# Performance work log

Hardware: AMD Instinct MI355X
Metric: run time of the kernel (lower is better)

## Reference

```python
import jax, jax.numpy as jnp
import numpy as np

N_NODES = 100000
IN_CH, HID_CH, OUT_CH = 128, 128, 64
N_EDGES = 1600000


def _gcn_conv(x, W, b, src, dst, num_nodes):
    """PyG GCNConv with gcn_norm(add_self_loops=True): adds one self-loop per
    node to the given edge set, symmetric deg^-1/2 normalization, then
    gather-scale-scatter of the linearly transformed features."""
    loop = jnp.arange(num_nodes)
    s = jnp.concatenate([src, loop])
    d = jnp.concatenate([dst, loop])
    # degree over targets (flow source_to_target), edge weights = 1
    deg = jax.ops.segment_sum(jnp.ones_like(s, x.dtype), d, num_segments=num_nodes)
    dinv = jnp.where(deg > 0, deg ** -0.5, 0.0)
    norm = dinv[s] * dinv[d]                      # [E']
    h = x @ W                                     # [N, out]
    msg = h[s] * norm[:, None]                    # [E', out] gather + scale
    out = jax.ops.segment_sum(msg, d, num_segments=num_nodes)  # scatter-add
    return out + b


def setup_inputs() -> dict:
    key = jax.random.key(0)
    k = jax.random.split(key, 6)
    x = jax.random.normal(k[0], (N_NODES, IN_CH), dtype=jnp.float32)
    edge_index = jax.random.randint(k[1], (2, N_EDGES), 0, N_NODES, dtype=jnp.int64)
    # Glorot-scale params
    W1 = jax.random.normal(k[2], (IN_CH, HID_CH), dtype=jnp.float32) * (2.0 / (IN_CH + HID_CH)) ** 0.5
    b1 = jnp.zeros((HID_CH,), dtype=jnp.float32)
    W2 = jax.random.normal(k[3], (HID_CH, OUT_CH), dtype=jnp.float32) * (2.0 / (HID_CH + OUT_CH)) ** 0.5
    b2 = jnp.zeros((OUT_CH,), dtype=jnp.float32)
    return {"x": x, "edge_index": edge_index, "W1": W1, "b1": b1, "W2": W2, "b2": b2}


def reference(x, edge_index, W1, b1, W2, b2):
    num_nodes = x.shape[0]
    loop = jnp.arange(num_nodes, dtype=edge_index.dtype)
    # wrapper-level add_self_loops (GCNConv adds another internally)
    src = jnp.concatenate([edge_index[0], loop])
    dst = jnp.concatenate([edge_index[1], loop])
    h = _gcn_conv(x, W1, b1, src, dst, num_nodes)
    h = jax.nn.relu(h)
    h = _gcn_conv(h, W2, b2, src, dst, num_nodes)
    return jax.nn.log_softmax(h, axis=1)
```

## Files before the change

### kernel.cpp

```cpp
#include <hip/hip_runtime.h>
#include <cstdint>
#include <cstddef>

#define IN_CH 128
#define HID_CH 128
#define OUT_CH 64
#define BSH 8
#define PB 4096
#define CAP 6144

typedef unsigned int uint32;
typedef unsigned char uchar;
typedef short bf16x8 __attribute__((ext_vector_type(8)));
typedef float f32x4 __attribute__((ext_vector_type(4)));
typedef float f32x2 __attribute__((ext_vector_type(2)));

static __device__ __forceinline__ unsigned short f2bf(float f) {
    uint32 u = __float_as_uint(f);
    u += 0x7fffu + ((u >> 16) & 1u);
    return (unsigned short)(u >> 16);
}

typedef const __attribute__((address_space(1))) char gch;
typedef __attribute__((address_space(3))) char lch;
static __device__ __forceinline__ void gload16(const void* g, void* l) {
    __builtin_amdgcn_global_load_lds((gch*)g, (lch*)l, 16, 0, 0);
}


__global__ __launch_bounds__(256) void part1_wtrans(
    const int* __restrict__ src, const int* __restrict__ dst,
    int* __restrict__ bcur, int2* __restrict__ pairBuf, int E, int NB, int gP,
    const float* __restrict__ W1, const float* __restrict__ W2,
    unsigned short* __restrict__ W1t, unsigned short* __restrict__ W2t) {
    if (blockIdx.x >= (uint32)gP) {
        int t = (blockIdx.x - gP) * 256 + threadIdx.x;
        if (t < 128 * 128) {
            int nc = t >> 7, k = t & 127;
            W1t[t] = f2bf(W1[k * 128 + nc]);
        }
        int u = t - 128 * 128;
        if (u >= 0 && u < 64 * 128) {
            int nc = u >> 7, k = u & 127;
            W2t[u] = f2bf(W2[k * 64 + nc]);
        }
        return;
    }
    __shared__ int2 pairs[PB];
    __shared__ int hist[512];
    __shared__ int base[512];
    int t = threadIdx.x;
    int e0 = blockIdx.x * PB;
    int cnt = min(PB, E - e0);
    for (int b = t; b < NB; b += 256) hist[b] = 0;
    __syncthreads();
    for (int i = t; i < cnt; i += 256) {
        int s = src[e0 + i], d = dst[e0 + i];
        pairs[i] = make_int2(s, d);
        atomicAdd(&hist[d >> BSH], 1);
    }
    __syncthreads();
    for (int b = t; b < NB; b += 256) {
        int h = hist[b];
        int gb = (h > 0) ? atomicAdd(&bcur[b], h) : 0;
        base[b] = b * CAP + gb;
        hist[b] = 0;
    }
    __syncthreads();
    for (int i = t; i < cnt; i += 256) {
        int2 p = pairs[i];
        int b = p.y >> BSH;
        int q = base[b] + atomicAdd(&hist[b], 1);
        pairBuf[q] = p;
    }
}

__global__ __launch_bounds__(256) void bucket_build(
    const int2* __restrict__ pairBuf, const int* __restrict__ bcur,
    int* __restrict__ rowptr, int* __restrict__ deg, float* __restrict__ dinv,
    int* __restrict__ csr, int N) {
    __shared__ int cnt[256];
    __shared__ int loc[256];
    int b = blockIdx.x, t = threadIdx.x;
    int start = b * CAP, end = start + bcur[b];
    cnt[t] = 0;
    __syncthreads();
    for (int i = start + t; i < end; i += 256)
        atomicAdd(&cnt[pairBuf[i].y & 255], 1);
    __syncthreads();
    int v = cnt[t];
    loc[t] = v;
    __syncthreads();
    for (int o = 1; o < 256; o <<= 1) {
        int add = (t >= o) ? loc[t - o] : 0;
        __syncthreads();
        loc[t] += add;
        __syncthreads();
    }
    int excl = loc[t] - v;
    int node = (b << BSH) + t;
    if (node < N) {
        rowptr[node] = start + excl;
        deg[node] = v;
        dinv[node] = rsqrtf((float)(v + 2));
    }
    __syncthreads();
    cnt[t] = excl;
    __syncthreads();
    for (int i = start + t; i < end; i += 256) {
        int2 p = pairBuf[i];
        int q = start + atomicAdd(&cnt[p.y & 255], 1);
        csr[q] = p.x;
    }
}


__global__ __launch_bounds__(256) void gemm1_mfma(
    const float* __restrict__ A, const unsigned short* __restrict__ Wt,
    const float* __restrict__ dinv, uchar* __restrict__ C, int n, int nTiles) {
    constexpr int NT = 8;
    __shared__ unsigned short Ws[128 * 136];
    __shared__ char As[64 * 512];

    const int t = threadIdx.x;

    for (int i = t; i < 128 * 16; i += 256) {
        int rr = i >> 4, sq = i & 15;
        *(uint4*)&Ws[rr * 136 + sq * 8] = *(const uint4*)(Wt + rr * 128 + sq * 8);
    }

    const int w = t >> 6, l = t & 63;
    const int q = l >> 4, r16 = l & 15;
    const int rw = w * 16 + r16;

    for (int tile = blockIdx.x; tile < nTiles; tile += gridDim.x) {
        const int row0 = tile * 64;

#pragma unroll
        for (int rnd = 0; rnd < 8; rnd++) {
            int p = rnd * 4096 + t * 16;
            int row = row0 + (p >> 9);
            int col = p & 511;
            gload16((const char*)A + (size_t)min(row, n - 1) * 512 + col, As + p);
        }
        __syncthreads();

        f32x4 acc[NT];
#pragma unroll
        for (int i = 0; i < NT; i++) acc[i] = (f32x4){0.f, 0.f, 0.f, 0.f};

#pragma unroll
        for (int s = 0; s < 4; s++) {
            const int k0 = s * 32 + q * 8;
            const float* Arow = (const float*)(As + rw * 512);
            float4 v0 = *(const float4*)(Arow + k0);
            float4 v1 = *(const float4*)(Arow + k0 + 4);
            bf16x8 xf;
            xf[0] = (short)f2bf(v0.x); xf[1] = (short)f2bf(v0.y);
            xf[2] = (short)f2bf(v0.z); xf[3] = (short)f2bf(v0.w);
            xf[4] = (short)f2bf(v1.x); xf[5] = (short)f2bf(v1.y);
            xf[6] = (short)f2bf(v1.z); xf[7] = (short)f2bf(v1.w);
#pragma unroll
            for (int nt = 0; nt < NT; nt++) {
                bf16x8 wf = *(const bf16x8*)&Ws[(nt * 16 + r16) * 136 + k0];
                acc[nt] = __builtin_amdgcn_mfma_f32_16x16x32_bf16(wf, xf, acc[nt], 0, 0, 0);
            }
        }

        const int node = row0 + rw;
        const bool nv = node < n;
        const float dv = dinv[min(node, n - 1)];
        uchar* Crow = C + (size_t)node * 128;
#pragma unroll
        for (int nt = 0; nt < NT; nt++) {
            int pk = 0;
            pk = __builtin_amdgcn_cvt_pk_fp8_f32(acc[nt][0] * dv, acc[nt][1] * dv, pk, false);
            pk = __builtin_amdgcn_cvt_pk_fp8_f32(acc[nt][2] * dv, acc[nt][3] * dv, pk, true);
            if (nv) *(uint32*)(Crow + nt * 16 + q * 4) = (uint32)pk;
        }
        __syncthreads();
    }
}


__global__ __launch_bounds__(256) void agg1_fused(
    const uchar* __restrict__ H, const int* __restrict__ csr,
    const int* __restrict__ rowptr, const int* __restrict__ deg,
    const float* __restrict__ dinv, const float* __restrict__ bias,
    const unsigned short* __restrict__ W2t, uchar* __restrict__ H2, int n) {
    __shared__ char stage[4][8192];
    __shared__ unsigned short tile[16 * 136];
    int t = threadIdx.x;
    int slot = t >> 4;
    int v = blockIdx.x * 16 + slot;
    int hl = t & 15;
    int gsel = t & 48;
    int w = t >> 6;
    int gg = (t >> 4) & 3;
    bool valid = v < n;
    int vc = valid ? v : 0;
    int base = rowptr[vc];
    int cnt = valid ? deg[vc] : 0;

    f32x2 A0 = (f32x2){0.f, 0.f}, A1 = A0, A2 = A0, A3 = A0;
    f32x2 B0 = A0, B1 = A0, B2 = A0, B3 = A0;

#define ACC128(h, s0, s1, s2, s3)                                   \
    {                                                               \
        s0 += __builtin_amdgcn_cvt_pk_f32_fp8((h).x, false);        \
        s1 += __builtin_amdgcn_cvt_pk_f32_fp8((h).x, true);         \
        s2 += __builtin_amdgcn_cvt_pk_f32_fp8((h).y, false);        \
        s3 += __builtin_amdgcn_cvt_pk_f32_fp8((h).y, true);         \
    }

    char* sl = stage[w];
    const char* rg = sl + gg * 256 + hl * 8;

    int ul = 0;
    if (hl < min(16, cnt)) ul = csr[base + hl];

    for (int j0 = 0; j0 < cnt; j0 += 16) {
        int nj = min(16, cnt - j0);
#pragma unroll
        for (int i = 0; i < 8; i++) {
            int j = i * 2 + (hl >> 3);
            int u = __shfl(ul, j | gsel);
            gload16(H + (((uint32)u << 7) + ((uint32)(hl & 7) << 4)),
                    sl + i * 1024);
        }
        int ul2 = 0;
        int j0n = j0 + 16;
        if (j0n < cnt && hl < min(16, cnt - j0n)) ul2 = csr[base + j0n + hl];
        asm volatile("s_waitcnt vmcnt(4)" ::: "memory");
        __builtin_amdgcn_sched_barrier(0);
#pragma unroll
        for (int j = 0; j < 8; j++) {
            if (j < nj) {
                uint2 h = *(const uint2*)(rg + (j >> 1) * 1024 + (j & 1) * 128);
                if (j & 1) { ACC128(h, B0, B1, B2, B3); }
                else       { ACC128(h, A0, A1, A2, A3); }
            }
        }
        asm volatile("s_waitcnt vmcnt(0)" ::: "memory");
        __builtin_amdgcn_sched_barrier(0);
#pragma unroll
        for (int j = 8; j < 16; j++) {
            if (j < nj) {
                uint2 h = *(const uint2*)(rg + (j >> 1) * 1024 + (j & 1) * 128);
                if (j & 1) { ACC128(h, B0, B1, B2, B3); }
                else       { ACC128(h, A0, A1, A2, A3); }
            }
        }
        ul = ul2;
    }
#undef ACC128

    const uint32 co = (uint32)(hl * 8);
    uint4 pk = make_uint4(0, 0, 0, 0);
    if (valid) {
        float dv = dinv[vc];
        uint2 hv = *(const uint2*)(H + (((uint32)vc << 7) + co));
        f32x2 s0 = __builtin_amdgcn_cvt_pk_f32_fp8(hv.x, false);
        f32x2 s1 = __builtin_amdgcn_cvt_pk_f32_fp8(hv.x, true);
        f32x2 s2 = __builtin_amdgcn_cvt_pk_f32_fp8(hv.y, false);
        f32x2 s3 = __builtin_amdgcn_cvt_pk_f32_fp8(hv.y, true);
        const f32x2* bp = (const f32x2*)(bias + hl * 8);
        f32x2 e0 = dv * ((A0 + B0) + 2.f * s0) + bp[0];
        f32x2 e1 = dv * ((A1 + B1) + 2.f * s1) + bp[1];
        f32x2 e2 = dv * ((A2 + B2) + 2.f * s2) + bp[2];
        f32x2 e3 = dv * ((A3 + B3) + 2.f * s3) + bp[3];
        float o0 = fmaxf(e0[0], 0.f), o1 = fmaxf(e0[1], 0.f);
        float o2 = fmaxf(e1[0], 0.f), o3 = fmaxf(e1[1], 0.f);
        float o4 = fmaxf(e2[0], 0.f), o5 = fmaxf(e2[1], 0.f);
        float o6 = fmaxf(e3[0], 0.f), o7 = fmaxf(e3[1], 0.f);
        pk.x = (uint32)f2bf(o0) | ((uint32)f2bf(o1) << 16);
        pk.y = (uint32)f2bf(o2) | ((uint32)f2bf(o3) << 16);
        pk.z = (uint32)f2bf(o4) | ((uint32)f2bf(o5) << 16);
        pk.w = (uint32)f2bf(o6) | ((uint32)f2bf(o7) << 16);
    }
    *(uint4*)&tile[slot * 136 + hl * 8] = pk;
    __syncthreads();

    const int l = t & 63;
    const int q = l >> 4, r16 = l & 15;
    f32x4 acc2 = (f32x4){0.f, 0.f, 0.f, 0.f};
#pragma unroll
    for (int s = 0; s < 4; s++) {
        const int k0 = s * 32 + q * 8;
        bf16x8 hf = *(const bf16x8*)&tile[r16 * 136 + k0];
        bf16x8 wf = *(const bf16x8*)(W2t + (size_t)(w * 16 + r16) * 128 + k0);
        acc2 = __builtin_amdgcn_mfma_f32_16x16x32_bf16(wf, hf, acc2, 0, 0, 0);
    }
    const int node = blockIdx.x * 16 + r16;
    if (node < n) {
        const float dv2 = dinv[node];
        int pk2 = 0;
        pk2 = __builtin_amdgcn_cvt_pk_fp8_f32(acc2[0] * dv2, acc2[1] * dv2, pk2, false);
        pk2 = __builtin_amdgcn_cvt_pk_fp8_f32(acc2[2] * dv2, acc2[3] * dv2, pk2, true);
        *(uint32*)(H2 + (size_t)node * 64 + w * 16 + q * 4) = (uint32)pk2;
    }
}

__global__ __launch_bounds__(256) void agg_lsm_64(
    const uchar* __restrict__ H, const int* __restrict__ csr,
    const int* __restrict__ rowptr, const int* __restrict__ deg,
    const float* __restrict__ dinv, const float* __restrict__ bias,
    float* __restrict__ out, int n) {
    __shared__ char stage[4][4096];
    int t = threadIdx.x;
    int v = blockIdx.x * 16 + (t >> 4);
    int hl = t & 15;
    int gsel = t & 48;
    int w = t >> 6;
    int gg = (t >> 4) & 3;
    bool valid = v < n;
    int vc = valid ? v : 0;
    int base = rowptr[vc];
    int cnt = valid ? deg[vc] : 0;
    const uint32 co = (uint32)(hl * 4);

    f32x2 A0 = (f32x2){0.f, 0.f}, A1 = A0, B0 = A0, B1 = A0;

#define ACC64(h, s0, s1)                                            \
    {                                                               \
        s0 += __builtin_amdgcn_cvt_pk_f32_fp8((h), false);          \
        s1 += __builtin_amdgcn_cvt_pk_f32_fp8((h), true);           \
    }

    char* sl = stage[w];
    const char* rg = sl + gg * 256 + hl * 4;

    int ul = 0;
    if (hl < min(16, cnt)) ul = csr[base + hl];

    for (int j0 = 0; j0 < cnt; j0 += 16) {
        int nj = min(16, cnt - j0);
#pragma unroll
        for (int i = 0; i < 4; i++) {
            int j = i * 4 + (hl >> 2);
            int u = __shfl(ul, j | gsel);
            gload16(H + (((uint32)u << 6) + ((uint32)(hl & 3) << 4)),
                    sl + i * 1024);
        }
        int ul2 = 0;
        int j0n = j0 + 16;
        if (j0n < cnt && hl < min(16, cnt - j0n)) ul2 = csr[base + j0n + hl];
        asm volatile("s_waitcnt vmcnt(2)" ::: "memory");
        __builtin_amdgcn_sched_barrier(0);
#pragma unroll
        for (int j = 0; j < 8; j++) {
            if (j < nj) {
                uint32 h = *(const uint32*)(rg + (j >> 2) * 1024 + (j & 3) * 64);
                if (j & 1) { ACC64(h, B0, B1); }
                else       { ACC64(h, A0, A1); }
            }
        }
        asm volatile("s_waitcnt vmcnt(0)" ::: "memory");
        __builtin_amdgcn_sched_barrier(0);
#pragma unroll
        for (int j = 8; j < 16; j++) {
            if (j < nj) {
                uint32 h = *(const uint32*)(rg + (j >> 2) * 1024 + (j & 3) * 64);
                if (j & 1) { ACC64(h, B0, B1); }
                else       { ACC64(h, A0, A1); }
            }
        }
        ul = ul2;
    }
#undef ACC64

    float dv = dinv[vc];
    uint32 hv = *(const uint32*)(H + (((uint32)vc << 6) + co));
    f32x2 s0 = __builtin_amdgcn_cvt_pk_f32_fp8(hv, false);
    f32x2 s1 = __builtin_amdgcn_cvt_pk_f32_fp8(hv, true);
    const f32x2* bp = (const f32x2*)(bias + hl * 4);
    f32x2 w0 = dv * ((A0 + B0) + 2.f * s0) + bp[0];
    f32x2 w1 = dv * ((A1 + B1) + 2.f * s1) + bp[1];
    float v0 = w0[0], v1 = w0[1], v2 = w1[0], v3 = w1[1];
    float m = fmaxf(fmaxf(v0, v1), fmaxf(v2, v3));
    for (int o = 8; o > 0; o >>= 1) m = fmaxf(m, __shfl_xor(m, o));
    float e = (__expf(v0 - m) + __expf(v1 - m)) + (__expf(v2 - m) + __expf(v3 - m));
    for (int o = 8; o > 0; o >>= 1) e += __shfl_xor(e, o);
    float ls = m + __logf(e);
    if (valid)
        *(float4*)(out + (size_t)vc * 64 + hl * 4) =
            make_float4(v0 - ls, v1 - ls, v2 - ls, v3 - ls);
}


extern "C" void kernel_launch(void* const* d_in, const int* in_sizes, int n_in,
                              void* d_out, int out_size, void* d_ws, size_t ws_size,
                              hipStream_t stream) {
    const float* x  = (const float*)d_in[0];
    const int*   ei = (const int*)d_in[1];
    const float* W1 = (const float*)d_in[2];
    const float* b1 = (const float*)d_in[3];
    const float* W2 = (const float*)d_in[4];
    const float* b2 = (const float*)d_in[5];
    float* out = (float*)d_out;

    const int N = in_sizes[0] / IN_CH;
    const int E = in_sizes[1] / 2;
    const int* src = ei;
    const int* dst = ei + E;
    const int NB = (N + 255) >> BSH;

    char* w = (char*)d_ws;
    size_t off = 0;
    auto alloc = [&](size_t bytes) -> char* {
        char* p = w + off;
        off = (off + bytes + 255) & ~(size_t)255;
        return p;
    };
    int*   deg    = (int*)alloc((size_t)N * 4);
    int*   rowptr = (int*)alloc((size_t)N * 4);
    int*   bcur   = (int*)alloc(512 * 4);
    float* dinv   = (float*)alloc((size_t)N * 4 + 1024);
    int*   csr    = (int*)alloc((size_t)NB * CAP * 4);
    unsigned short* W1t = (unsigned short*)alloc(128 * 128 * 2);
    unsigned short* W2t = (unsigned short*)alloc(64 * 128 * 2);
    uchar* H1  = (uchar*)alloc((size_t)N * HID_CH);
    char*  scratch = alloc((size_t)NB * CAP * 8);
    uchar* H2  = (uchar*)scratch;
    int2*  pairBuf = (int2*)scratch;

    hipMemsetAsync(bcur, 0, 512 * 4, stream);

    int gP = (E + PB - 1) / PB;

    part1_wtrans<<<gP + 96, 256, 0, stream>>>(src, dst, bcur, pairBuf, E, NB, gP,
                                              W1, W2, W1t, W2t);
    bucket_build<<<NB, 256, 0, stream>>>(pairBuf, bcur, rowptr, deg, dinv, csr, N);

    const int nTiles = (N + 63) / 64;
    const int gG = min(nTiles, 512);
    gemm1_mfma<<<gG, 256, 0, stream>>>(x, W1t, dinv, H1, N, nTiles);
    agg1_fused<<<(N + 15) / 16, 256, 0, stream>>>(H1, csr, rowptr, deg, dinv, b1, W2t, H2, N);
    agg_lsm_64<<<(N + 15) / 16, 256, 0, stream>>>(H2, csr, rowptr, deg, dinv, b2, out, N);
}
```

Baseline: 217.2 us.

## Replace bucketed CSR build with global-atomic degree count, scan and scatter

Replaces the two-pass bucket-sort CSR construction (local histogram into padded pairBuf, then a per-bucket sort) with a global atomic degree count, a two-level prefix scan, and a direct scatter that uses per-node atomic cursors. The dinv array is dropped and recomputed with rsqrt from the degree wherever it is needed, and rowptr is derived from bucket base plus the post-scatter cursor minus degree. This removes the 8-byte pair staging buffer and the padded CAP layout, at the cost of 1.6M global atomics on node counters, which can contend, and two more kernel launches.

```diff
diff --git a/kernel.cpp b/kernel.cpp
--- a/kernel.cpp
+++ b/kernel.cpp
@@ -5,9 +5,6 @@
 #define IN_CH 128
 #define HID_CH 128
 #define OUT_CH 64
-#define BSH 8
-#define PB 4096
-#define CAP 6144
 
 typedef unsigned int uint32;
 typedef unsigned char uchar;
@@ -28,13 +25,12 @@
 }
 
 
-__global__ __launch_bounds__(256) void part1_wtrans(
-    const int* __restrict__ src, const int* __restrict__ dst,
-    int* __restrict__ bcur, int2* __restrict__ pairBuf, int E, int NB, int gP,
+__global__ __launch_bounds__(256) void deg_wtrans(
+    const int* __restrict__ dst, int* __restrict__ deg, int E, int gD,
     const float* __restrict__ W1, const float* __restrict__ W2,
     unsigned short* __restrict__ W1t, unsigned short* __restrict__ W2t) {
-    if (blockIdx.x >= (uint32)gP) {
-        int t = (blockIdx.x - gP) * 256 + threadIdx.x;
+    if (blockIdx.x >= (uint32)gD) {
+        int t = (blockIdx.x - gD) * 256 + threadIdx.x;
         if (t < 128 * 128) {
             int nc = t >> 7, k = t & 127;
             W1t[t] = f2bf(W1[k * 128 + nc]);
@@ -46,78 +42,67 @@
         }
         return;
     }
-    __shared__ int2 pairs[PB];
-    __shared__ int hist[512];
-    __shared__ int base[512];
-    int t = threadIdx.x;
-    int e0 = blockIdx.x * PB;
-    int cnt = min(PB, E - e0);
-    for (int b = t; b < NB; b += 256) hist[b] = 0;
-    __syncthreads();
-    for (int i = t; i < cnt; i += 256) {
-        int s = src[e0 + i], d = dst[e0 + i];
-        pairs[i] = make_int2(s, d);
-        atomicAdd(&hist[d >> BSH], 1);
-    }
-    __syncthreads();
-    for (int b = t; b < NB; b += 256) {
-        int h = hist[b];
-        int gb = (h > 0) ? atomicAdd(&bcur[b], h) : 0;
-        base[b] = b * CAP + gb;
-        hist[b] = 0;
-    }
-    __syncthreads();
-    for (int i = t; i < cnt; i += 256) {
-        int2 p = pairs[i];
-        int b = p.y >> BSH;
-        int q = base[b] + atomicAdd(&hist[b], 1);
-        pairBuf[q] = p;
-    }
-}
-
-__global__ __launch_bounds__(256) void bucket_build(
-    const int2* __restrict__ pairBuf, const int* __restrict__ bcur,
-    int* __restrict__ rowptr, int* __restrict__ deg, float* __restrict__ dinv,
-    int* __restrict__ csr, int N) {
-    __shared__ int cnt[256];
-    __shared__ int loc[256];
+    int i0 = blockIdx.x * 256 + threadIdx.x;
+    int stride = gD * 256;
+    for (int i = i0; i < E; i += stride)
+        atomicAdd(&deg[dst[i]], 1);
+}
+
+__global__ __launch_bounds__(256) void scan_local(
+    const int* __restrict__ deg, int* __restrict__ rowloc,
+    int* __restrict__ bsum, int N) {
+    __shared__ int s[256];
     int b = blockIdx.x, t = threadIdx.x;
-    int start = b * CAP, end = start + bcur[b];
-    cnt[t] = 0;
-    __syncthreads();
-    for (int i = start + t; i < end; i += 256)
-        atomicAdd(&cnt[pairBuf[i].y & 255], 1);
-    __syncthreads();
-    int v = cnt[t];
-    loc[t] = v;
+    int node = (b << 8) + t;
+    int v = (node < N) ? deg[node] : 0;
+    s[t] = v;
     __syncthreads();
     for (int o = 1; o < 256; o <<= 1) {
-        int add = (t >= o) ? loc[t - o] : 0;
-        __syncthreads();
-        loc[t] += add;
-        __syncthreads();
-    }
-    int excl = loc[t] - v;
-    int node = (b << BSH) + t;
-    if (node < N) {
-        rowptr[node] = start + excl;
-        deg[node] = v;
-        dinv[node] = rsqrtf((float)(v + 2));
-    }
+        int a = (t >= o) ? s[t - o] : 0;
+        __syncthreads();
+        s[t] += a;
+        __syncthreads();
+    }
+    if (node < N) rowloc[node] = s[t] - v;
+    if (t == 255) bsum[b] = s[t];
+}
+
+__global__ void bscan2(const int* __restrict__ bsum, int* __restrict__ bbase, int NB) {
+    __shared__ int s[512];
+    int t = threadIdx.x;
+    int v = (t < NB) ? bsum[t] : 0;
+    s[t] = v;
     __syncthreads();
-    cnt[t] = excl;
+    for (int o = 1; o < 512; o <<= 1) {
+        int a = (t >= o) ? s[t - o] : 0;
+        __syncthreads();
+        s[t] += a;
+        __syncthreads();
+    }
+    if (t < NB) bbase[t] = s[t] - v;
+}
+
+__global__ __launch_bounds__(256) void scatter(
+    const int* __restrict__ src, const int* __restrict__ dst,
+    const int* __restrict__ bbase, int* __restrict__ rowloc,
+    int* __restrict__ csr, int E, int NB) {
+    __shared__ int bb[512];
+    int t = threadIdx.x;
+    for (int b = t; b < NB; b += 256) bb[b] = bbase[b];
     __syncthreads();
-    for (int i = start + t; i < end; i += 256) {
-        int2 p = pairBuf[i];
-        int q = start + atomicAdd(&cnt[p.y & 255], 1);
-        csr[q] = p.x;
+    int i0 = blockIdx.x * 256 + t;
+    int stride = gridDim.x * 256;
+    for (int i = i0; i < E; i += stride) {
+        int s = src[i], d = dst[i];
+        int q = bb[d >> 8] + atomicAdd(&rowloc[d], 1);
+        csr[q] = s;
     }
 }
 
 
 __global__ __launch_bounds__(256) void gemm1_mfma(
     const float* __restrict__ A, const unsigned short* __restrict__ Wt,
-    const float* __restrict__ dinv, uchar* __restrict__ C, int n, int nTiles) {
+    const int* __restrict__ degp, uchar* __restrict__ C, int n, int nTiles) {
     constexpr int NT = 8;
     __shared__ unsigned short Ws[128 * 136];
     __shared__ char As[64 * 512];
@@ -169,7 +154,8 @@
 
         const int node = row0 + rw;
         const bool nv = node < n;
-        const float dv = dinv[min(node, n - 1)];
+        const int dgv = degp[min(node, n - 1)];
+        const float dv = rsqrtf((float)(dgv + 2));
         uchar* Crow = C + (size_t)node * 128;
 #pragma unroll
         for (int nt = 0; nt < NT; nt++) {
@@ -185,8 +171,8 @@
 
 __global__ __launch_bounds__(256) void agg1_fused(
     const uchar* __restrict__ H, const int* __restrict__ csr,
-    const int* __restrict__ rowptr, const int* __restrict__ deg,
-    const float* __restrict__ dinv, const float* __restrict__ bias,
+    const int* __restrict__ rowloc, const int* __restrict__ bbase,
+    const int* __restrict__ deg, const float* __restrict__ bias,
     const unsigned short* __restrict__ W2t, uchar* __restrict__ H2, int n) {
     __shared__ char stage[4][8192];
     __shared__ unsigned short tile[16 * 136];
@@ -199,8 +185,8 @@
     int gg = (t >> 4) & 3;
     bool valid = v < n;
     int vc = valid ? v : 0;
-    int base = rowptr[vc];
     int cnt = valid ? deg[vc] : 0;
+    int base = bbase[vc >> 8] + rowloc[vc] - cnt;
 
     f32x2 A0 = (f32x2){0.f, 0.f}, A1 = A0, A2 = A0, A3 = A0;
     f32x2 B0 = A0, B1 = A0, B2 = A0, B3 = A0;
@@ -258,7 +244,7 @@
     const uint32 co = (uint32)(hl * 8);
     uint4 pk = make_uint4(0, 0, 0, 0);
     if (valid) {
-        float dv = dinv[vc];
+        float dv = rsqrtf((float)(cnt + 2));
         uint2 hv = *(const uint2*)(H + (((uint32)vc << 7) + co));
         f32x2 s0 = __builtin_amdgcn_cvt_pk_f32_fp8(hv.x, false);
         f32x2 s1 = __builtin_amdgcn_cvt_pk_f32_fp8(hv.x, true);
@@ -293,7 +279,7 @@
     }
     const int node = blockIdx.x * 16 + r16;
     if (node < n) {
-        const float dv2 = dinv[node];
+        const float dv2 = rsqrtf((float)(deg[node] + 2));
         int pk2 = 0;
         pk2 = __builtin_amdgcn_cvt_pk_fp8_f32(acc2[0] * dv2, acc2[1] * dv2, pk2, false);
         pk2 = __builtin_amdgcn_cvt_pk_fp8_f32(acc2[2] * dv2, acc2[3] * dv2, pk2, true);
@@ -303,8 +289,8 @@
 
 __global__ __launch_bounds__(256) void agg_lsm_64(
     const uchar* __restrict__ H, const int* __restrict__ csr,
-    const int* __restrict__ rowptr, const int* __restrict__ deg,
-    const float* __restrict__ dinv, const float* __restrict__ bias,
+    const int* __restrict__ rowloc, const int* __restrict__ bbase,
+    const int* __restrict__ deg, const float* __restrict__ bias,
     float* __restrict__ out, int n) {
     __shared__ char stage[4][4096];
     int t = threadIdx.x;
@@ -315,8 +301,8 @@
     int gg = (t >> 4) & 3;
     bool valid = v < n;
     int vc = valid ? v : 0;
-    int base = rowptr[vc];
     int cnt = valid ? deg[vc] : 0;
+    int base = bbase[vc >> 8] + rowloc[vc] - cnt;
     const uint32 co = (uint32)(hl * 4);
 
     f32x2 A0 = (f32x2){0.f, 0.f}, A1 = A0, B0 = A0, B1 = A0;
@@ -369,7 +355,7 @@
     }
 #undef ACC64
 
-    float dv = dinv[vc];
+    float dv = rsqrtf((float)(cnt + 2));
     uint32 hv = *(const uint32*)(H + (((uint32)vc << 6) + co));
     f32x2 s0 = __builtin_amdgcn_cvt_pk_f32_fp8(hv, false);
     f32x2 s1 = __builtin_amdgcn_cvt_pk_f32_fp8(hv, true);
@@ -403,7 +389,7 @@
     const int E = in_sizes[1] / 2;
     const int* src = ei;
     const int* dst = ei + E;
-    const int NB = (N + 255) >> BSH;
+    const int NB = (N + 255) >> 8;
 
     char* w = (char*)d_ws;
     size_t off = 0;
@@ -413,28 +399,26 @@
         return p;
     };
     int*   deg    = (int*)alloc((size_t)N * 4);
-    int*   rowptr = (int*)alloc((size_t)N * 4);
-    int*   bcur   = (int*)alloc(512 * 4);
-    float* dinv   = (float*)alloc((size_t)N * 4 + 1024);
-    int*   csr    = (int*)alloc((size_t)NB * CAP * 4);
+    int*   rowloc = (int*)alloc((size_t)N * 4);
+    int*   bsum   = (int*)alloc(512 * 4);
+    int*   bbase  = (int*)alloc(512 * 4);
+    int*   csr    = (int*)alloc((size_t)E * 4);
     unsigned short* W1t = (unsigned short*)alloc(128 * 128 * 2);
     unsigned short* W2t = (unsigned short*)alloc(64 * 128 * 2);
     uchar* H1  = (uchar*)alloc((size_t)N * HID_CH);
-    char*  scratch = alloc((size_t)NB * CAP * 8);
-    uchar* H2  = (uchar*)scratch;
-    int2*  pairBuf = (int2*)scratch;
-
-    hipMemsetAsync(bcur, 0, 512 * 4, stream);
-
-    int gP = (E + PB - 1) / PB;
-
-    part1_wtrans<<<gP + 96, 256, 0, stream>>>(src, dst, bcur, pairBuf, E, NB, gP,
-                                              W1, W2, W1t, W2t);
-    bucket_build<<<NB, 256, 0, stream>>>(pairBuf, bcur, rowptr, deg, dinv, csr, N);
+    uchar* H2  = (uchar*)alloc((size_t)N * OUT_CH);
+
+    hipMemsetAsync(deg, 0, (size_t)N * 4, stream);
+
+    const int gD = 1024;
+    deg_wtrans<<<gD + 96, 256, 0, stream>>>(dst, deg, E, gD, W1, W2, W1t, W2t);
+    scan_local<<<NB, 256, 0, stream>>>(deg, rowloc, bsum, N);
+    bscan2<<<1, 512, 0, stream>>>(bsum, bbase, NB);
+    scatter<<<1024, 256, 0, stream>>>(src, dst, bbase, rowloc, csr, E, NB);
 
     const int nTiles = (N + 63) / 64;
     const int gG = min(nTiles, 512);
-    gemm1_mfma<<<gG, 256, 0, stream>>>(x, W1t, dinv, H1, N, nTiles);
-    agg1_fused<<<(N + 15) / 16, 256, 0, stream>>>(H1, csr, rowptr, deg, dinv, b1, W2t, H2, N);
-    agg_lsm_64<<<(N + 15) / 16, 256, 0, stream>>>(H2, csr, rowptr, deg, dinv, b2, out, N);
-}
+    gemm1_mfma<<<gG, 256, 0, stream>>>(x, W1t, deg, H1, N, nTiles);
+    agg1_fused<<<(N + 15) / 16, 256, 0, stream>>>(H1, csr, rowloc, bbase, deg, b1, W2t, H2, N);
+    agg_lsm_64<<<(N + 15) / 16, 256, 0, stream>>>(H2, csr, rowloc, bbase, deg, b2, out, N);
+}
```

New measurement: 375.7 us. 1.73x slower.
